# Optimization experiments

Measured on AMD Instinct MI355X. Metric: run time of the kernel, lower is better.

## Reference

```python
import jax, jax.numpy as jnp
import numpy as np

N = 50000      # nodes
E = 800000     # edges (before self loops)
DIN = 128      # input_dim
H = 128        # hidden_dim
DOUT = 64      # output_dim
G = 64         # graphs in batch
EATTR = 16     # edge_attr dim (unused by math, kept for signature fidelity)


def _conv_params(key, din, h, scale=0.05):
    ks = jax.random.split(key, 6)
    return dict(
        lin_w=jax.random.normal(ks[0], (din, h), dtype=jnp.float32) * scale,
        lin_b=jnp.zeros((h,), jnp.float32),
        w1=jax.random.normal(ks[1], (2 * h, h), dtype=jnp.float32) * scale,
        b1=jnp.zeros((h,), jnp.float32),
        w2=jax.random.normal(ks[2], (h, h), dtype=jnp.float32) * scale,
        b2=jnp.zeros((h,), jnp.float32),
    )


def setup_inputs() -> dict:
    key = jax.random.key(0)
    ks = jax.random.split(key, 10)
    inp = {
        'x': jax.random.normal(ks[0], (N, DIN), dtype=jnp.float32),
        'edge_index': jax.random.randint(ks[1], (2, E), 0, N),
        'edge_attr': jax.random.normal(ks[2], (E, EATTR), dtype=jnp.float32),
        'batch': jnp.sort(jax.random.randint(ks[3], (N,), 0, G)),
    }
    p1 = _conv_params(ks[4], DIN, H)
    p2 = _conv_params(ks[5], H, H)
    p3 = _conv_params(ks[6], H, H)
    for i, p in enumerate((p1, p2, p3), start=1):
        for k, v in p.items():
            inp[f'c{i}_{k}'] = v
    inp['out_w'] = jax.random.normal(ks[7], (H, DOUT), dtype=jnp.float32) * 0.05
    inp['out_b'] = jnp.zeros((DOUT,), jnp.float32)
    return inp


def mpnn_conv(x, src, dst, lin_w, lin_b, w1, b1, w2, b2):
    # x: [N, din] -> h: [N, H]
    n = x.shape[0]
    h = x @ lin_w + lin_b
    loop = jnp.arange(n)
    s = jnp.concatenate([src, loop])   # x_j (source) indices, self loops appended
    d = jnp.concatenate([dst, loop])   # x_i (target) indices
    z = jnp.concatenate([h[d], h[s]], axis=-1)          # [E+N, 2H]  (cat[x_i, x_j])
    m = jax.nn.relu(z @ w1 + b1) @ w2 + b2              # [E+N, H]
    return jax.ops.segment_sum(m, d, num_segments=n)    # aggr='add' at targets


def reference(x, edge_index, edge_attr, batch,
              c1_lin_w, c1_lin_b, c1_w1, c1_b1, c1_w2, c1_b2,
              c2_lin_w, c2_lin_b, c2_w1, c2_b1, c2_w2, c2_b2,
              c3_lin_w, c3_lin_b, c3_w1, c3_b1, c3_w2, c3_b2,
              out_w, out_b):
    src, dst = edge_index[0], edge_index[1]
    h = jax.nn.relu(mpnn_conv(x, src, dst, c1_lin_w, c1_lin_b, c1_w1, c1_b1, c1_w2, c1_b2))
    h = jax.nn.relu(mpnn_conv(h, src, dst, c2_lin_w, c2_lin_b, c2_w1, c2_b1, c2_w2, c2_b2))
    h = jax.nn.relu(mpnn_conv(h, src, dst, c3_lin_w, c3_lin_b, c3_w1, c3_b1, c3_w2, c3_b2))
    # global_mean_pool over graphs
    sums = jax.ops.segment_sum(h, batch, num_segments=G)                       # [G, H]
    cnts = jax.ops.segment_sum(jnp.ones((h.shape[0],), h.dtype), batch, num_segments=G)
    pooled = sums / jnp.maximum(cnts, 1.0)[:, None]
    return pooled @ out_w + out_b
```

## Files before the change

### kernel.cpp

```cpp
#include <hip/hip_runtime.h>
#include <hip/hip_bf16.h>


typedef _Float16 f16_t;
typedef f16_t f16x2 __attribute__((ext_vector_type(2)));
typedef f16_t f16x8 __attribute__((ext_vector_type(8)));
typedef float f32x4 __attribute__((ext_vector_type(4)));
typedef float f32x2v __attribute__((ext_vector_type(2)));
typedef unsigned int u32;
typedef unsigned short u16;
typedef unsigned char u8;

__device__ __forceinline__ float f16lo(u32 v) {
    return (float)__builtin_bit_cast(f16_t, (u16)(v & 0xffff));
}
__device__ __forceinline__ float f16hi(u32 v) {
    return (float)__builtin_bit_cast(f16_t, (u16)(v >> 16));
}
__device__ __forceinline__ u16 f16b(float x) { return __builtin_bit_cast(u16, (f16_t)x); }
__device__ __forceinline__ u32 f16pack(float x, float y) {
    return (u32)f16b(x) | ((u32)f16b(y) << 16);
}

typedef __attribute__((address_space(1))) void gvoid_t;
typedef __attribute__((address_space(3))) void lvoid_t;
__device__ __forceinline__ void glds16(const void* g, void* l) {
    __builtin_amdgcn_global_load_lds((gvoid_t*)g, (lvoid_t*)l, 16, 0, 0);
}

struct PrepArgs {
    const float* x; f16_t* xb; int totalx;
    const int* ei; int E;
    int* hist; int nbk; int NB;
    const float* lin_w[3]; const float* lin_b[3];
    const float* w1[3]; const float* b1[3]; const float* w2[3];
    f16_t* linw16;
    f16_t* w1T;
    f16_t* W2t;
    float* bias256c;
};

__global__ __launch_bounds__(256) void prep_kernel(PrepArgs A, int nConvB) {
    __shared__ union { int hist[512]; u16 T16[128 * 130]; } shm;
    const int b = blockIdx.x, tid = threadIdx.x;
    const int nTr = 9, nLw = 48, nBias = 3;
    if (b < nTr) {
        int layer = b / 3, which = b % 3;
        const float* src; f16_t* dst;
        if (which == 0)      { src = A.w1[layer];          dst = A.w1T + layer * 32768; }
        else if (which == 1) { src = A.w1[layer] + 16384;  dst = A.w1T + layer * 32768 + 16384; }
        else                 { src = A.w2[layer];          dst = A.W2t + layer * 16384; }
#pragma unroll
        for (int it = 0; it < 16; ++it) {
            int idx = it * 1024 + tid * 4;
            int r = idx >> 7, c = idx & 127;
            float4 v = *(const float4*)(src + idx);
            *(u32*)&shm.T16[r * 130 + c] = f16pack(v.x, v.y);
            *(u32*)&shm.T16[r * 130 + c + 2] = f16pack(v.z, v.w);
        }
        __syncthreads();
#pragma unroll
        for (int it = 0; it < 32; ++it) {
            int o = it * 256 + tid;
            int j = o >> 6, c = (o & 63) * 2;
            u32 w = (u32)shm.T16[c * 130 + j] | ((u32)shm.T16[(c + 1) * 130 + j] << 16);
            ((u32*)dst)[o] = w;
        }
        return;
    }
    if (b < nTr + nLw) {
        int i = (b - nTr) * 1024 + tid * 4;
        int layer = i >> 14, off = i & 16383;
        float4 v = *(const float4*)(A.lin_w[layer] + off);
        *(uint2*)(A.linw16 + i) = make_uint2(f16pack(v.x, v.y), f16pack(v.z, v.w));
        return;
    }
    if (b < nTr + nLw + nBias) {
        int layer = b - nTr - nLw;
        int j = tid;
        const float* w1p = A.w1[layer];
        const float* wcol = (j < 128) ? (w1p + j) : (w1p + 16384 + (j - 128));
        const float* lbp = A.lin_b[layer];
        float s = (j < 128) ? A.b1[layer][j] : 0.f;
        for (int c = 0; c < 128; ++c) s += lbp[c] * wcol[c * 128];
        A.bias256c[layer * 256 + j] = s;
        return;
    }
    if (b < nTr + nLw + nBias + A.NB) {
        const int bb = b - nTr - nLw - nBias;
        const int nbk = A.nbk, E = A.E;
        for (int i = tid; i < nbk; i += 256) shm.hist[i] = 0;
        __syncthreads();
        const int chunk = (E + A.NB - 1) / A.NB;
        const int e0 = bb * chunk, e1 = min(E, e0 + chunk);
        for (int e = e0 + tid; e < e1; e += 256) atomicAdd(&shm.hist[A.ei[E + e] >> 7], 1);
        __syncthreads();
        for (int i = tid; i < nbk; i += 256) A.hist[(size_t)bb * nbk + i] = shm.hist[i];
        return;
    }
    int i = ((b - nTr - nLw - nBias - A.NB) * 256 + tid) * 4;
    if (i >= A.totalx) return;
    float4 v = *(const float4*)(A.x + i);
    *(uint2*)(A.xb + i) = make_uint2(f16pack(v.x, v.y), f16pack(v.z, v.w));
}

__global__ __launch_bounds__(256) void hscan_kernel(int* __restrict__ hist,
                                                    int* __restrict__ bcnt, int nbk, int NB) {
    __shared__ int sh[256];
    const int b = blockIdx.x, t = threadIdx.x;
    int run = 0;
    for (int c0 = 0; c0 < NB; c0 += 256) {
        int idx = c0 + t;
        int v = (idx < NB) ? hist[(size_t)idx * nbk + b] : 0;
        sh[t] = v;
        __syncthreads();
#pragma unroll
        for (int o = 1; o < 256; o <<= 1) {
            int u = (t >= o) ? sh[t - o] : 0;
            __syncthreads();
            sh[t] += u;
            __syncthreads();
        }
        if (idx < NB) hist[(size_t)idx * nbk + b] = run + sh[t] - v;
        int tot = sh[255];
        __syncthreads();
        run += tot;
    }
    if (t == 0) bcnt[b] = run;
}

__global__ __launch_bounds__(256) void scat_kernel(const int* __restrict__ ei,
                                                   const int* __restrict__ hist,
                                                   u32* __restrict__ bbuf, int E, int NB,
                                                   int nbk, int cap) {
    __shared__ int basep[512];
    __shared__ int cnt2[512];
    const int bb = blockIdx.x, t = threadIdx.x;
    for (int i = t; i < nbk; i += 256) {
        basep[i] = hist[(size_t)bb * nbk + i];
        cnt2[i] = 0;
    }
    __syncthreads();
    const int chunk = (E + NB - 1) / NB;
    const int e0 = bb * chunk, e1 = min(E, e0 + chunk);
    for (int e = e0 + t; e < e1; e += 256) {
        int dst = ei[E + e], src = ei[e];
        int bkt = dst >> 7;
        int r = atomicAdd(&cnt2[bkt], 1);
        int pp = basep[bkt] + r;
        if (pp < cap) bbuf[(size_t)bkt * cap + pp] = ((u32)(dst & 127) << 16) | (u32)src;
    }
}

__global__ __launch_bounds__(128) void part2_kernel(const u32* __restrict__ bbuf,
                                                    const int* __restrict__ bcnt,
                                                    int* __restrict__ row_ptr,
                                                    float* __restrict__ cntp1f,
                                                    int* __restrict__ bsumB, int cap, int N) {
    __shared__ int ldeg[128];
    __shared__ int sh[128];
    const int b = blockIdx.x, t = threadIdx.x;
    ldeg[t] = 0;
    __syncthreads();
    const int cnt = min(bcnt[b], cap);
    const u32* p = bbuf + (size_t)b * cap;
    for (int i = t; i < cnt; i += 128) atomicAdd(&ldeg[p[i] >> 16], 1);
    __syncthreads();
    int d = ldeg[t];
    sh[t] = d;
    __syncthreads();
#pragma unroll
    for (int o = 1; o < 128; o <<= 1) {
        int u = (t >= o) ? sh[t - o] : 0;
        __syncthreads();
        sh[t] += u;
        __syncthreads();
    }
    int node = (b << 7) + t;
    if (node < N) {
        row_ptr[node] = sh[t] - d;
        cntp1f[node] = (float)(d + 1);
    }
    if (t == 127) bsumB[b] = sh[127];
}

__global__ __launch_bounds__(512) void scanb_kernel(const int* __restrict__ bsumB,
                                                    int* __restrict__ bbase,
                                                    int* __restrict__ row_ptr, int nbk, int N) {
    __shared__ int sh[512];
    const int t = threadIdx.x;
    int v = (t < nbk) ? bsumB[t] : 0;
    sh[t] = v;
    __syncthreads();
#pragma unroll
    for (int o = 1; o < 512; o <<= 1) {
        int u = (t >= o) ? sh[t - o] : 0;
        __syncthreads();
        sh[t] += u;
        __syncthreads();
    }
    if (t < nbk) bbase[t] = sh[t] - v;
    if (t == 511) row_ptr[N] = sh[511];
}

__global__ __launch_bounds__(128) void part3_kernel(const u32* __restrict__ bbuf,
                                                    const int* __restrict__ bcnt,
                                                    const int* __restrict__ bbase,
                                                    int* __restrict__ row_ptr,
                                                    u16* __restrict__ colarr, int cap, int N) {
    __shared__ int lcur[128];
    const int b = blockIdx.x, t = threadIdx.x;
    const int node = (b << 7) + t;
    const int bb = bbase[b];
    int rp = 0;
    if (node < N) {
        rp = row_ptr[node] + bb;
        row_ptr[node] = rp;
    }
    lcur[t] = rp;
    __syncthreads();
    const int cnt = min(bcnt[b], cap);
    const u32* p = bbuf + (size_t)b * cap;
    for (int i = t; i < cnt; i += 128) {
        u32 en = p[i];
        int addr = atomicAdd(&lcur[en >> 16], 1);
        colarr[addr] = (u16)(en & 0xffffu);
    }
}

__device__ __forceinline__ void gemm_tile(const f16_t* __restrict__ X,
                                          const f16_t* __restrict__ Wt,
                                          f16_t* __restrict__ Y, int N,
                                          int ldc, int row0) {
    __shared__ f16_t sX[128 * 128];
    __shared__ f16_t sW[128 * 128];
    const int tid = threadIdx.x;
    const int wave = tid >> 6, lane = tid & 63;
#pragma unroll
    for (int it = 0; it < 8; ++it) {
        int idx = it * 256 + tid;
        int r = idx >> 4, c8 = idx & 15;
        int gr = row0 + r;
        if (gr >= N) gr = 0;
        glds16(X + (size_t)gr * 128 + ((c8 ^ (r & 7)) * 8),
               sX + (size_t)(it * 256 + (wave << 6)) * 8);
    }
#pragma unroll
    for (int it = 0; it < 8; ++it) {
        int idx = it * 256 + tid;
        int r = idx >> 4, c8 = idx & 15;
        glds16(Wt + (size_t)r * 128 + ((c8 ^ (r & 7)) * 8),
               sW + (size_t)(it * 256 + (wave << 6)) * 8);
    }
    __syncthreads();
    const int m = lane & 15, q = lane >> 4;
    const int sw = m & 7;
    f32x4 acc[2][8];
#pragma unroll
    for (int rt = 0; rt < 2; ++rt)
#pragma unroll
        for (int t = 0; t < 8; ++t) acc[rt][t] = (f32x4){0.f, 0.f, 0.f, 0.f};
#pragma unroll
    for (int kk = 0; kk < 4; ++kk) {
        const int g = (kk * 4 + q) ^ sw;
        f16x8 a0 = *(const f16x8*)(&sX[(wave * 32 + m) * 128 + g * 8]);
        f16x8 a1 = *(const f16x8*)(&sX[(wave * 32 + 16 + m) * 128 + g * 8]);
#pragma unroll
        for (int t = 0; t < 8; ++t) {
            f16x8 bfr = *(const f16x8*)(&sW[(t * 16 + m) * 128 + g * 8]);
            acc[0][t] = __builtin_amdgcn_mfma_f32_16x16x32_f16(a0, bfr, acc[0][t], 0, 0, 0);
            acc[1][t] = __builtin_amdgcn_mfma_f32_16x16x32_f16(a1, bfr, acc[1][t], 0, 0, 0);
        }
    }
#pragma unroll
    for (int t = 0; t < 8; ++t) {
        int col = t * 16 + m;
#pragma unroll
        for (int rt = 0; rt < 2; ++rt) {
#pragma unroll
            for (int j = 0; j < 4; ++j) {
                int r = row0 + wave * 32 + rt * 16 + q * 4 + j;
                if (r < N) Y[(size_t)r * ldc + col] = (f16_t)acc[rt][t][j];
            }
        }
    }
}

__global__ __launch_bounds__(256) void compose_kernel(const f16_t* __restrict__ w1T,
                                                      const f16_t* __restrict__ linw16,
                                                      f16_t* __restrict__ W12ct) {
    int layer = blockIdx.x >> 1, rb = blockIdx.x & 1;
    gemm_tile(w1T + layer * 32768, linw16 + layer * 16384, W12ct + layer * 32768, 256, 128,
              rb * 128);
}

template <int NT>
__global__ __launch_bounds__(512, 1) void gemm_persist(
    const f16_t* __restrict__ X, const f16_t* __restrict__ Wt,
    const float* __restrict__ bias, const float* __restrict__ bias2,
    const float* __restrict__ rowscale, f16_t* __restrict__ Y, u8* __restrict__ Y8,
    int N, int relu_flag, int ntiles) {
    __shared__ f16_t sW[NT * 16 * 128];
    __shared__ f16_t sX[2][128 * 128];
    const int tid = threadIdx.x;
    const int wave = tid >> 6, lane = tid & 63;
    const int m = lane & 15, q = lane >> 4, sw = m & 7;
    constexpr int NR = (NT == 16) ? 2 : 1;
    const int rb0 = (NT == 16) ? ((wave & 3) * 32) : (wave * 16);
    const int chalf = (NT == 16) ? (wave >> 2) : 0;

#pragma unroll
    for (int it = 0; it < NT / 2; ++it) {
        int idx = it * 512 + tid;
        int r = idx >> 4, c8 = idx & 15;
        glds16(Wt + (size_t)r * 128 + ((c8 ^ (r & 7)) * 8),
               sW + (size_t)(it * 512 + (wave << 6)) * 8);
    }
    float bvv[8], b2vv[8];
#pragma unroll
    for (int t2 = 0; t2 < 8; ++t2) {
        int colb = chalf * 128 + t2 * 16 + m;
        bvv[t2] = bias ? bias[colb] : 0.f;
        b2vv[t2] = bias2 ? bias2[colb] : 0.f;
    }
    int t = blockIdx.x;
    {
        int row0 = t * 128;
#pragma unroll
        for (int it = 0; it < 4; ++it) {
            int idx = it * 512 + tid;
            int r = idx >> 4, c8 = idx & 15;
            int gr = row0 + r;
            if (gr >= N) gr = 0;
            glds16(X + (size_t)gr * 128 + ((c8 ^ (r & 7)) * 8),
                   sX[0] + (size_t)(it * 512 + (wave << 6)) * 8);
        }
    }
    __syncthreads();
    int cur = 0;
    for (; t < ntiles; t += gridDim.x) {
        const int row0 = t * 128;
        const int tn = t + gridDim.x;
        f16_t* sXc = sX[cur];
        if (tn < ntiles) {
            const int r0n = tn * 128;
            f16_t* sXn = sX[cur ^ 1];
#pragma unroll
            for (int it = 0; it < 4; ++it) {
                int idx = it * 512 + tid;
                int r = idx >> 4, c8 = idx & 15;
                int gr = r0n + r;
                if (gr >= N) gr = 0;
                glds16(X + (size_t)gr * 128 + ((c8 ^ (r & 7)) * 8),
                       sXn + (size_t)(it * 512 + (wave << 6)) * 8);
            }
        }
        f32x4 acc[NR][8];
#pragma unroll
        for (int rt = 0; rt < NR; ++rt)
#pragma unroll
            for (int t2 = 0; t2 < 8; ++t2) acc[rt][t2] = (f32x4){0.f, 0.f, 0.f, 0.f};
#pragma unroll
        for (int kk = 0; kk < 4; ++kk) {
            const int g = (kk * 4 + q) ^ sw;
            f16x8 a0 = *(const f16x8*)(&sXc[(rb0 + m) * 128 + g * 8]);
            f16x8 a1{};
            if constexpr (NR == 2) a1 = *(const f16x8*)(&sXc[(rb0 + 16 + m) * 128 + g * 8]);
#pragma unroll
            for (int t2 = 0; t2 < 8; ++t2) {
                f16x8 bfr =
                    *(const f16x8*)(&sW[(size_t)(chalf * 128 + t2 * 16 + m) * 128 + g * 8]);
                acc[0][t2] = __builtin_amdgcn_mfma_f32_16x16x32_f16(a0, bfr, acc[0][t2], 0, 0, 0);
                if constexpr (NR == 2)
                    acc[1][t2] =
                        __builtin_amdgcn_mfma_f32_16x16x32_f16(a1, bfr, acc[1][t2], 0, 0, 0);
            }
        }
        if (NT == 16) __syncthreads();
        f16_t* region = sXc + wave * 16 * 128;
#pragma unroll
        for (int rt = 0; rt < NR; ++rt) {
            float rs[4];
#pragma unroll
            for (int j = 0; j < 4; ++j) {
                int gr = row0 + rb0 + rt * 16 + q * 4 + j;
                rs[j] = (bias2 && gr < N) ? rowscale[gr] : 0.f;
            }
#pragma unroll
            for (int t2 = 0; t2 < 8; ++t2) {
#pragma unroll
                for (int j = 0; j < 4; ++j) {
                    int rl2 = q * 4 + j;
                    float v = acc[rt][t2][j] + bvv[t2];
                    if (bias2) v += rs[j] * b2vv[t2];
                    if (relu_flag) v = fmaxf(v, 0.f);
                    region[rl2 * 128 + ((t2 * 16 + m) ^ ((rl2 & 4) << 3))] = (f16_t)v;
                }
            }
#pragma unroll
            for (int it2 = 0; it2 < 4; ++it2) {
                int i = it2 * 64 + lane;
                int rl = i >> 4, c8 = i & 15;
                int gr = row0 + rb0 + rt * 16 + rl;
                const f16_t* rp = &region[rl * 128 + ((c8 ^ (rl & 4)) * 8)];
                if (NT == 16 && chalf == 1) {
                    const u32* p = (const u32*)rp;
                    u32 lo = __builtin_amdgcn_cvt_pk_fp8_f32(f16lo(p[0]), f16hi(p[0]), 0u, false);
                    lo = __builtin_amdgcn_cvt_pk_fp8_f32(f16lo(p[1]), f16hi(p[1]), lo, true);
                    u32 hi = __builtin_amdgcn_cvt_pk_fp8_f32(f16lo(p[2]), f16hi(p[2]), 0u, false);
                    hi = __builtin_amdgcn_cvt_pk_fp8_f32(f16lo(p[3]), f16hi(p[3]), hi, true);
                    if (gr < N) *(uint2*)(Y8 + (size_t)gr * 128 + c8 * 8) = make_uint2(lo, hi);
                } else {
                    uint4 v4 = *(const uint4*)rp;
                    if (gr < N) *(uint4*)(Y + (size_t)gr * 128 + c8 * 8) = v4;
                }
            }
        }
        __syncthreads();
        cur ^= 1;
    }
}

__global__ __launch_bounds__(256) void gather_kernel(const f16_t* __restrict__ aArr,
                                                     const u8* __restrict__ b8,
                                                     const int* __restrict__ row_ptr,
                                                     const u16* __restrict__ colarr,
                                                     f16_t* __restrict__ q, int N) {
    int wid = (blockIdx.x * 256 + threadIdx.x) >> 6;
    int lane = threadIdx.x & 63;
    if (wid >= N) return;
    const int g = lane >> 4, l = lane & 15;
    uint4 A = ((const uint4*)aArr)[(size_t)wid * 16 + l];
    float a0 = f16lo(A.x), a1 = f16hi(A.x), a2 = f16lo(A.y), a3 = f16hi(A.y);
    float a4 = f16lo(A.z), a5 = f16hi(A.z), a6 = f16lo(A.w), a7 = f16hi(A.w);
    float c0 = 0.f, c1 = 0.f, c2 = 0.f, c3 = 0.f, c4 = 0.f, c5 = 0.f, c6 = 0.f, c7 = 0.f;
    const uint2* b8u = (const uint2*)b8;
    auto accum = [&](uint2 B) {
        f32x2v p0 = __builtin_amdgcn_cvt_pk_f32_fp8(B.x, false);
        f32x2v p1 = __builtin_amdgcn_cvt_pk_f32_fp8(B.x, true);
        f32x2v p2 = __builtin_amdgcn_cvt_pk_f32_fp8(B.y, false);
        f32x2v p3 = __builtin_amdgcn_cvt_pk_f32_fp8(B.y, true);
        c0 += fmaxf(a0 + p0.x, 0.f); c1 += fmaxf(a1 + p0.y, 0.f);
        c2 += fmaxf(a2 + p1.x, 0.f); c3 += fmaxf(a3 + p1.y, 0.f);
        c4 += fmaxf(a4 + p2.x, 0.f); c5 += fmaxf(a5 + p2.y, 0.f);
        c6 += fmaxf(a6 + p3.x, 0.f); c7 += fmaxf(a7 + p3.y, 0.f);
    };
    if (g == 0) accum(b8u[(size_t)wid * 16 + l]);
    const int e0 = row_ptr[wid], e1 = row_ptr[wid + 1];
    for (int e = e0; e < e1; e += 16) {
#pragma unroll
        for (int s = 0; s < 4; ++s) {
            int idx = e + s * 4 + g;
            int src = colarr[min(idx, e1 - 1)];
            uint2 B = b8u[(size_t)src * 16 + l];
            if (idx < e1) accum(B);
        }
    }
#pragma unroll
    for (int off = 16; off < 64; off <<= 1) {
        c0 += __shfl_xor(c0, off); c1 += __shfl_xor(c1, off);
        c2 += __shfl_xor(c2, off); c3 += __shfl_xor(c3, off);
        c4 += __shfl_xor(c4, off); c5 += __shfl_xor(c5, off);
        c6 += __shfl_xor(c6, off); c7 += __shfl_xor(c7, off);
    }
    if (g == 0) {
        uint4 o;
        o.x = f16pack(c0, c1); o.y = f16pack(c2, c3);
        o.z = f16pack(c4, c5); o.w = f16pack(c6, c7);
        ((uint4*)q)[(size_t)wid * 16 + l] = o;
    }
}

__global__ __launch_bounds__(256) void pool_kernel(const f16_t* __restrict__ agg,
                                                   const int* __restrict__ batch,
                                                   float* __restrict__ pooled,
                                                   int* __restrict__ cntg, int N) {
    int wid = (blockIdx.x * 256 + threadIdx.x) >> 6;
    int lane = threadIdx.x & 63;
    int n0 = wid * 8;
    if (n0 >= N) return;
    int n1 = min(n0 + 8, N);
    const u32* au = (const u32*)agg;
    int gcur = batch[n0];
    float sx = 0.f, sy = 0.f;
    int cnt = 0;
    for (int n = n0; n < n1; ++n) {
        int g = batch[n];
        if (g != gcur) {
            atomicAdd(&pooled[gcur * 128 + lane * 2], sx);
            atomicAdd(&pooled[gcur * 128 + lane * 2 + 1], sy);
            if (lane == 0) atomicAdd(&cntg[gcur], cnt);
            gcur = g; sx = 0.f; sy = 0.f; cnt = 0;
        }
        u32 v = au[(size_t)n * 64 + lane];
        sx += f16lo(v);
        sy += f16hi(v);
        ++cnt;
    }
    atomicAdd(&pooled[gcur * 128 + lane * 2], sx);
    atomicAdd(&pooled[gcur * 128 + lane * 2 + 1], sy);
    if (lane == 0) atomicAdd(&cntg[gcur], cnt);
}

__global__ __launch_bounds__(256) void final_kernel(const float* __restrict__ pooled,
                                                    const int* __restrict__ cntg,
                                                    const float* __restrict__ out_w,
                                                    const float* __restrict__ out_b,
                                                    float* __restrict__ out) {
    __shared__ float red[256];
    const int g = blockIdx.x, tid = threadIdx.x;
    const int o = tid & 63, part = tid >> 6;
    float s = 0.f;
#pragma unroll
    for (int kk = 0; kk < 32; ++kk) {
        int k = part * 32 + kk;
        s += pooled[g * 128 + k] * out_w[k * 64 + o];
    }
    red[tid] = s;
    __syncthreads();
    if (part == 0) {
        float c = fmaxf((float)cntg[g], 1.0f);
        float tot = red[o] + red[o + 64] + red[o + 128] + red[o + 192];
        out[g * 64 + o] = tot / c + out_b[o];
    }
}

extern "C" void kernel_launch(void* const* d_in, const int* in_sizes, int n_in, void* d_out,
                              int out_size, void* d_ws, size_t ws_size, hipStream_t stream) {
    const float* x = (const float*)d_in[0];
    const int* ei = (const int*)d_in[1];
    const int* batch = (const int*)d_in[3];
    const float* cw[3][6];
    for (int l = 0; l < 3; ++l)
        for (int j = 0; j < 6; ++j) cw[l][j] = (const float*)d_in[4 + l * 6 + j];
    const float* out_w = (const float*)d_in[22];
    const float* out_b = (const float*)d_in[23];
    float* out = (float*)d_out;

    const int N = in_sizes[0] / 128;
    const int E = in_sizes[1] / 2;
    const int G = out_size / 64;
    const int nbk = (N + 127) >> 7;
    const int NB = 416;
    const int cap = E / nbk + 512;

    char* base = (char*)d_ws;
    size_t off = 0;
    auto alloc = [&](size_t b) { size_t o = off; off += (b + 255) & ~(size_t)255; return o; };
    float* pooled = (float*)(base + alloc((size_t)G * 128 * 4));
    int* cntg = (int*)(base + alloc((size_t)G * 4));
    const size_t zero_bytes = off;
    int* hist = (int*)(base + alloc((size_t)NB * nbk * 4));
    int* bcnt = (int*)(base + alloc((size_t)nbk * 4));
    int* bsumB = (int*)(base + alloc((size_t)nbk * 4));
    int* bbase = (int*)(base + alloc((size_t)nbk * 4));
    int* row_ptr = (int*)(base + alloc((size_t)(N + 1) * 4));
    float* cntp1f = (float*)(base + alloc((size_t)N * 4));
    u16* colarr = (u16*)(base + alloc((size_t)E * 2));
    u32* bbuf = (u32*)(base + alloc((size_t)nbk * cap * 4));
    f16_t* xb = (f16_t*)(base + alloc((size_t)N * 128 * 2));
    f16_t* q = (f16_t*)(base + alloc((size_t)N * 128 * 2));
    f16_t* aArr = (f16_t*)(base + alloc((size_t)N * 128 * 2));
    u8* b8 = (u8*)(base + alloc((size_t)N * 128));
    f16_t* linw16 = (f16_t*)(base + alloc(3 * 16384 * 2));
    f16_t* w1T = (f16_t*)(base + alloc(3 * 32768 * 2));
    f16_t* W12ct = (f16_t*)(base + alloc(3 * 32768 * 2));
    f16_t* W2t = (f16_t*)(base + alloc(3 * 16384 * 2));
    float* bias256c = (float*)(base + alloc(3 * 256 * 4));
    (void)ws_size; (void)n_in;

    hipMemsetAsync(d_ws, 0, zero_bytes, stream);

    PrepArgs pa;
    pa.x = x; pa.xb = xb; pa.totalx = N * 128;
    pa.ei = ei; pa.E = E;
    pa.hist = hist; pa.nbk = nbk; pa.NB = NB;
    for (int l = 0; l < 3; ++l) {
        pa.lin_w[l] = cw[l][0]; pa.lin_b[l] = cw[l][1];
        pa.w1[l] = cw[l][2]; pa.b1[l] = cw[l][3]; pa.w2[l] = cw[l][4];
    }
    pa.linw16 = linw16; pa.w1T = w1T; pa.W2t = W2t; pa.bias256c = bias256c;
    const int nConvB = (N * 128 / 4 + 255) / 256;
    prep_kernel<<<9 + 48 + 3 + NB + nConvB, 256, 0, stream>>>(pa, nConvB);

    compose_kernel<<<6, 256, 0, stream>>>(w1T, linw16, W12ct);

    hscan_kernel<<<nbk, 256, 0, stream>>>(hist, bcnt, nbk, NB);
    scat_kernel<<<NB, 256, 0, stream>>>(ei, hist, bbuf, E, NB, nbk, cap);
    part2_kernel<<<nbk, 128, 0, stream>>>(bbuf, bcnt, row_ptr, cntp1f, bsumB, cap, N);
    scanb_kernel<<<1, 512, 0, stream>>>(bsumB, bbase, row_ptr, nbk, N);
    part3_kernel<<<nbk, 128, 0, stream>>>(bbuf, bcnt, bbase, row_ptr, colarr, cap, N);

    const int ntiles = (N + 127) >> 7;
    const int pgrid = (ntiles < 256) ? ntiles : 256;
    const f16_t* Xin = xb;
    for (int l = 0; l < 3; ++l) {
        gemm_persist<16><<<pgrid, 512, 0, stream>>>(Xin, W12ct + l * 32768,
                                                    bias256c + l * 256, nullptr, nullptr,
                                                    aArr, b8, N, 0, ntiles);
        gather_kernel<<<(N * 64 + 255) / 256, 256, 0, stream>>>(aArr, b8, row_ptr, colarr, q, N);
        gemm_persist<8><<<pgrid, 512, 0, stream>>>(q, W2t + l * 16384, nullptr, cw[l][5],
                                                   cntp1f, xb, nullptr, N, 1, ntiles);
        Xin = xb;
    }

    pool_kernel<<<((N + 7) / 8 * 64 + 255) / 256, 256, 0, stream>>>(Xin, batch, pooled, cntg, N);
    final_kernel<<<G, 256, 0, stream>>>(pooled, cntg, out_w, out_b, out);
}
```

Baseline: 413.6 us.

## Precompute graph segment offsets and pool per graph with block reduction

A new branch in the prep kernel computes per-graph start offsets from the sorted batch array. With these offsets the pooling kernel assigns 8 blocks per graph, reduces within each block through shared memory, and issues far fewer global float atomics. The final kernel derives node counts from the offsets instead of a separately atomically accumulated count array. This relies on batch being sorted, which the reference guarantees.

```diff
diff --git a/kernel.cpp b/kernel.cpp
--- a/kernel.cpp
+++ b/kernel.cpp
@@ -32,6 +32,7 @@
     const float* x; f16_t* xb; int totalx;
     const int* ei; int E;
     int* hist; int nbk; int NB;
+    const int* batch; int* gstart; int N; int G; int nBat;
     const float* lin_w[3]; const float* lin_b[3];
     const float* w1[3]; const float* b1[3]; const float* w2[3];
     f16_t* linw16;
@@ -98,7 +99,22 @@
         for (int i = tid; i < nbk; i += 256) A.hist[(size_t)bb * nbk + i] = shm.hist[i];
         return;
     }
-    int i = ((b - nTr - nLw - nBias - A.NB) * 256 + tid) * 4;
+    if (b < nTr + nLw + nBias + A.NB + A.nBat) {
+        int n = (b - nTr - nLw - nBias - A.NB) * 256 + tid;
+        if (n >= A.N) return;
+        int b1 = A.batch[n];
+        if (n == 0) {
+            for (int g = 0; g <= b1; ++g) A.gstart[g] = 0;
+        } else {
+            int b0 = A.batch[n - 1];
+            if (b0 != b1)
+                for (int g = b0 + 1; g <= b1; ++g) A.gstart[g] = n;
+        }
+        if (n == A.N - 1)
+            for (int g = b1 + 1; g <= A.G; ++g) A.gstart[g] = A.N;
+        return;
+    }
+    int i = ((b - nTr - nLw - nBias - A.NB - A.nBat) * 256 + tid) * 4;
     if (i >= A.totalx) return;
     float4 v = *(const float4*)(A.x + i);
     *(uint2*)(A.xb + i) = make_uint2(f16pack(v.x, v.y), f16pack(v.z, v.w));
@@ -472,38 +488,37 @@
 }
 
 __global__ __launch_bounds__(256) void pool_kernel(const f16_t* __restrict__ agg,
-                                                   const int* __restrict__ batch,
-                                                   float* __restrict__ pooled,
-                                                   int* __restrict__ cntg, int N) {
-    int wid = (blockIdx.x * 256 + threadIdx.x) >> 6;
-    int lane = threadIdx.x & 63;
-    int n0 = wid * 8;
-    if (n0 >= N) return;
-    int n1 = min(n0 + 8, N);
+                                                   const int* __restrict__ gstart,
+                                                   float* __restrict__ pooled) {
+    __shared__ float red[4][128];
+    const int g = blockIdx.x >> 3, part = blockIdx.x & 7;
+    const int tid = threadIdx.x, wave = tid >> 6, lane = tid & 63;
+    const int lo = gstart[g], hi = gstart[g + 1];
+    const int cnt = hi - lo;
+    const int len = (cnt + 7) >> 3;
+    const int n0 = lo + part * len, n1 = min(hi, n0 + len);
     const u32* au = (const u32*)agg;
-    int gcur = batch[n0];
     float sx = 0.f, sy = 0.f;
-    int cnt = 0;
-    for (int n = n0; n < n1; ++n) {
-        int g = batch[n];
-        if (g != gcur) {
-            atomicAdd(&pooled[gcur * 128 + lane * 2], sx);
-            atomicAdd(&pooled[gcur * 128 + lane * 2 + 1], sy);
-            if (lane == 0) atomicAdd(&cntg[gcur], cnt);
-            gcur = g; sx = 0.f; sy = 0.f; cnt = 0;
-        }
+#pragma unroll 4
+    for (int n = n0 + wave; n < n1; n += 4) {
         u32 v = au[(size_t)n * 64 + lane];
         sx += f16lo(v);
         sy += f16hi(v);
-        ++cnt;
-    }
-    atomicAdd(&pooled[gcur * 128 + lane * 2], sx);
-    atomicAdd(&pooled[gcur * 128 + lane * 2 + 1], sy);
-    if (lane == 0) atomicAdd(&cntg[gcur], cnt);
+    }
+    red[wave][lane * 2] = sx;
+    red[wave][lane * 2 + 1] = sy;
+    __syncthreads();
+    if (wave == 0) {
+        float a = red[0][lane * 2] + red[1][lane * 2] + red[2][lane * 2] + red[3][lane * 2];
+        float b = red[0][lane * 2 + 1] + red[1][lane * 2 + 1] + red[2][lane * 2 + 1] +
+                  red[3][lane * 2 + 1];
+        atomicAdd(&pooled[g * 128 + lane * 2], a);
+        atomicAdd(&pooled[g * 128 + lane * 2 + 1], b);
+    }
 }
 
 __global__ __launch_bounds__(256) void final_kernel(const float* __restrict__ pooled,
-                                                    const int* __restrict__ cntg,
+                                                    const int* __restrict__ gstart,
                                                     const float* __restrict__ out_w,
                                                     const float* __restrict__ out_b,
                                                     float* __restrict__ out) {
@@ -519,7 +534,7 @@
     red[tid] = s;
     __syncthreads();
     if (part == 0) {
-        float c = fmaxf((float)cntg[g], 1.0f);
+        float c = fmaxf((float)(gstart[g + 1] - gstart[g]), 1.0f);
         float tot = red[o] + red[o + 64] + red[o + 128] + red[o + 192];
         out[g * 64 + o] = tot / c + out_b[o];
     }
@@ -543,13 +558,14 @@
     const int nbk = (N + 127) >> 7;
     const int NB = 416;
     const int cap = E / nbk + 512;
+    const int nBat = (N + 255) / 256;
 
     char* base = (char*)d_ws;
     size_t off = 0;
     auto alloc = [&](size_t b) { size_t o = off; off += (b + 255) & ~(size_t)255; return o; };
     float* pooled = (float*)(base + alloc((size_t)G * 128 * 4));
-    int* cntg = (int*)(base + alloc((size_t)G * 4));
     const size_t zero_bytes = off;
+    int* gstart = (int*)(base + alloc((size_t)(G + 1) * 4));
     int* hist = (int*)(base + alloc((size_t)NB * nbk * 4));
     int* bcnt = (int*)(base + alloc((size_t)nbk * 4));
     int* bsumB = (int*)(base + alloc((size_t)nbk * 4));
@@ -575,13 +591,14 @@
     pa.x = x; pa.xb = xb; pa.totalx = N * 128;
     pa.ei = ei; pa.E = E;
     pa.hist = hist; pa.nbk = nbk; pa.NB = NB;
+    pa.batch = batch; pa.gstart = gstart; pa.N = N; pa.G = G; pa.nBat = nBat;
     for (int l = 0; l < 3; ++l) {
         pa.lin_w[l] = cw[l][0]; pa.lin_b[l] = cw[l][1];
         pa.w1[l] = cw[l][2]; pa.b1[l] = cw[l][3]; pa.w2[l] = cw[l][4];
     }
     pa.linw16 = linw16; pa.w1T = w1T; pa.W2t = W2t; pa.bias256c = bias256c;
     const int nConvB = (N * 128 / 4 + 255) / 256;
-    prep_kernel<<<9 + 48 + 3 + NB + nConvB, 256, 0, stream>>>(pa, nConvB);
+    prep_kernel<<<9 + 48 + 3 + NB + nBat + nConvB, 256, 0, stream>>>(pa, nConvB);
 
     compose_kernel<<<6, 256, 0, stream>>>(w1T, linw16, W12ct);
 
@@ -604,6 +621,6 @@
         Xin = xb;
     }
 
-    pool_kernel<<<((N + 7) / 8 * 64 + 255) / 256, 256, 0, stream>>>(Xin, batch, pooled, cntg, N);
-    final_kernel<<<G, 256, 0, stream>>>(pooled, cntg, out_w, out_b, out);
-}
+    pool_kernel<<<G * 8, 256, 0, stream>>>(Xin, gstart, pooled);
+    final_kernel<<<G, 256, 0, stream>>>(pooled, gstart, out_w, out_b, out);
+}
```

Result: faster. 379.6 us (-8.2%).
